# Performance work log

Measured on AMD Instinct MI355X. Metric: run time of the kernel, lower is better.

Reference implementation:

```python
import jax, jax.numpy as jnp
import numpy as np

D_MODEL = 96
EXPAND = 2.0
D_INNER = int(EXPAND * D_MODEL)  # 192
D_STATE = 1
DT_RANK = 6  # ceil(96/16)
K = 4
B, H, W = 4, 128, 128
L = H * W


def setup_inputs() -> dict:
    key = jax.random.key(0)
    ks = jax.random.split(key, 12)
    x = jax.random.normal(ks[0], (B, D_MODEL, H, W), dtype=jnp.float32)
    # 4 per-direction scan permutations of L and their inverses
    scan_ids = jnp.stack([jax.random.permutation(jax.random.fold_in(ks[1], k), L) for k in range(K)]).astype(jnp.int32)
    inverse_ids = jnp.argsort(scan_ids, axis=1).astype(jnp.int32)
    in_proj_w = jax.random.normal(ks[2], (D_INNER, D_MODEL), dtype=jnp.float32) * (1.0 / np.sqrt(D_MODEL))
    conv_w = jax.random.normal(ks[3], (D_INNER, 1, 3, 3), dtype=jnp.float32) * (1.0 / 3.0)
    conv_b = jax.random.normal(ks[4], (D_INNER,), dtype=jnp.float32) * 0.02
    x_proj_weight = jax.random.normal(ks[5], (K, DT_RANK + 2 * D_STATE, D_INNER), dtype=jnp.float32) * (1.0 / np.sqrt(D_INNER))
    dt_projs_weight = 0.1 * jax.random.uniform(ks[6], (K, D_INNER, DT_RANK), dtype=jnp.float32)
    dt_projs_bias = 0.1 * jax.random.uniform(ks[7], (K, D_INNER), dtype=jnp.float32)
    A_logs = jnp.zeros((K * D_INNER, D_STATE), dtype=jnp.float32)
    Ds = jnp.ones((K * D_INNER,), dtype=jnp.float32)
    out_proj_w = jax.random.normal(ks[8], (D_MODEL, D_INNER), dtype=jnp.float32) * (1.0 / np.sqrt(D_INNER))
    return {"x": x, "scan_ids": scan_ids, "inverse_ids": inverse_ids,
            "in_proj_w": in_proj_w, "conv_w": conv_w, "conv_b": conv_b,
            "x_proj_weight": x_proj_weight, "dt_projs_weight": dt_projs_weight,
            "dt_projs_bias": dt_projs_bias, "A_logs": A_logs, "Ds": Ds,
            "out_proj_w": out_proj_w}


def _selective_scan(u, delta, A, Bs, Cs, Ds, delta_bias):
    # u, delta: (B,K,D,L); A: (K,D,N); Bs, Cs: (B,K,N,L); Ds: (K,D); delta_bias: (K,D)
    delta = jax.nn.softplus(delta + delta_bias[None, :, :, None])  # (B,K,D,L)
    a = jnp.exp(delta[:, :, :, None, :] * A[None, :, :, :, None])  # (B,K,D,N,L)
    bu = delta[:, :, :, None, :] * Bs[:, :, None, :, :] * u[:, :, :, None, :]  # (B,K,D,N,L)

    def combine(lhs, rhs):
        aL, bL = lhs
        aR, bR = rhs
        return aR * aL, aR * bL + bR

    _, h = jax.lax.associative_scan(combine, (a, bu), axis=-1)  # h: (B,K,D,N,L)
    y = jnp.einsum('bknl,bkdnl->bkdl', Cs, h) + Ds[None, :, :, None] * u
    return y


def reference(x, scan_ids, inverse_ids, in_proj_w, conv_w, conv_b, x_proj_weight,
              dt_projs_weight, dt_projs_bias, A_logs, Ds, out_proj_w):
    Bsz, _, Hh, Ww = x.shape
    Ll = Hh * Ww
    # in_proj (1x1 conv == linear over channels)
    x = jnp.einsum('oc,bchw->bohw', in_proj_w, x)
    # depthwise 3x3 conv, padding SAME
    x = jax.lax.conv_general_dilated(x, conv_w, (1, 1), 'SAME',
                                     dimension_numbers=('NCHW', 'OIHW', 'NCHW'),
                                     feature_group_count=D_INNER)
    x = x + conv_b[None, :, None, None]
    x = jax.nn.silu(x)
    # 4-direction gather: (B,D,L) -> (B,K,D,L)
    xf = x.reshape(Bsz, D_INNER, Ll)
    xs = jnp.transpose(xf[:, :, scan_ids], (0, 2, 1, 3))  # (B,K,D,L)
    # input-dependent projections
    x_dbl = jnp.einsum('bkdl,kcd->bkcl', xs, x_proj_weight)
    dts, Bm, Cm = jnp.split(x_dbl, [DT_RANK, DT_RANK + D_STATE], axis=2)
    dts = jnp.einsum('bkrl,kdr->bkdl', dts, dt_projs_weight)
    A = -jnp.exp(A_logs.astype(jnp.float32)).reshape(K, D_INNER, D_STATE)
    ys = _selective_scan(xs.astype(jnp.float32), dts.astype(jnp.float32), A,
                         Bm.astype(jnp.float32), Cm.astype(jnp.float32),
                         Ds.astype(jnp.float32).reshape(K, D_INNER),
                         dt_projs_bias.astype(jnp.float32))  # (B,K,D,L)
    # inverse scatter per direction (gather with inverse permutation), then sum
    yinv = jnp.take_along_axis(ys, inverse_ids[None, :, None, :].astype(jnp.int32), axis=-1)
    y = jnp.sum(yinv, axis=1).reshape(Bsz, D_INNER, Hh, Ww)
    y = jax.nn.gelu(y)
    out = jnp.einsum('oc,bchw->bohw', out_proj_w, y)
    return out
```

## Files before the change

kernel.cpp:

```cpp
#include <hip/hip_runtime.h>
#include <math.h>

#define BATCH 4
#define HH 128
#define WWW 128
#define LLEN (HH*WWW)
#define CIN 96
#define DI 192
#define KDIR 4
#define NCH 512
#define PCH 32

__global__ __launch_bounds__(256) void k_inproj(const float* __restrict__ x,
                                                const float* __restrict__ w,
                                                float* __restrict__ t0) {
    __shared__ float xin[CIN * 64];
    __shared__ float wt[CIN * 65];
    int bid = blockIdx.x;
    int b = bid >> 8;
    int l0 = (bid & 255) << 6;
    int t = threadIdx.x;
    for (int i = 0; i < 24; ++i) {
        int idx = t + i * 256;
        int c = idx >> 6, l = idx & 63;
        xin[c * 64 + l] = x[((size_t)(b * CIN + c)) * LLEN + l0 + l];
    }
    int o_lane = t & 63;
    int lgrp = t >> 6;
    for (int ot = 0; ot < 3; ++ot) {
        __syncthreads();
        for (int i = 0; i < 24; ++i) {
            int idx = t + i * 256;
            int o = idx / 96, c = idx - o * 96;
            wt[c * 65 + o] = w[(ot * 64 + o) * 96 + c];
        }
        __syncthreads();
        float4 acc4[4];
        #pragma unroll
        for (int i = 0; i < 4; ++i) acc4[i] = make_float4(0.f, 0.f, 0.f, 0.f);
        int lb = lgrp * 16;
        for (int c = 0; c < CIN; ++c) {
            float wv = wt[c * 65 + o_lane];
            const float4* xv = reinterpret_cast<const float4*>(&xin[c * 64 + lb]);
            #pragma unroll
            for (int i = 0; i < 4; ++i) {
                float4 xx = xv[i];
                acc4[i].x += wv * xx.x; acc4[i].y += wv * xx.y;
                acc4[i].z += wv * xx.z; acc4[i].w += wv * xx.w;
            }
        }
        int o = ot * 64 + o_lane;
        #pragma unroll
        for (int i = 0; i < 4; ++i) {
            t0[((size_t)(b * LLEN) + l0 + lb + i * 4 + 0) * DI + o] = acc4[i].x;
            t0[((size_t)(b * LLEN) + l0 + lb + i * 4 + 1) * DI + o] = acc4[i].y;
            t0[((size_t)(b * LLEN) + l0 + lb + i * 4 + 2) * DI + o] = acc4[i].z;
            t0[((size_t)(b * LLEN) + l0 + lb + i * 4 + 3) * DI + o] = acc4[i].w;
        }
    }
}

__global__ __launch_bounds__(192) void k_dwconv(const float* __restrict__ t0,
                                                const float* __restrict__ cw,
                                                const float* __restrict__ cb,
                                                float* __restrict__ xf) {
    int bid = blockIdx.x;
    int wt = (bid & 15) << 3;
    int h  = (bid >> 4) & (HH - 1);
    int b  = bid >> 11;
    int d  = threadIdx.x;
    float acc[8];
    float bias = cb[d];
    #pragma unroll
    for (int j = 0; j < 8; ++j) acc[j] = bias;
    #pragma unroll
    for (int kh = 0; kh < 3; ++kh) {
        int hh = h + kh - 1;
        if (hh < 0 || hh >= HH) continue;
        float w0v = cw[d * 9 + kh * 3 + 0];
        float w1v = cw[d * 9 + kh * 3 + 1];
        float w2v = cw[d * 9 + kh * 3 + 2];
        const float* rowp = t0 + ((size_t)(b * LLEN) + hh * WWW) * DI + d;
        float v[10];
        #pragma unroll
        for (int j = 0; j < 10; ++j) {
            int ww = wt + j - 1;
            v[j] = (ww < 0 || ww >= WWW) ? 0.f : rowp[(size_t)ww * DI];
        }
        #pragma unroll
        for (int j = 0; j < 8; ++j)
            acc[j] += w0v * v[j] + w1v * v[j + 1] + w2v * v[j + 2];
    }
    size_t outbase = ((size_t)(b * LLEN) + h * WWW + wt) * DI + d;
    #pragma unroll
    for (int j = 0; j < 8; ++j) {
        float aa = acc[j];
        float s = aa * __builtin_amdgcn_rcpf(1.f + __expf(-aa));
        xf[outbase + (size_t)j * DI] = s;
    }
}

__global__ __launch_bounds__(256) void k_proj(const float* __restrict__ xf,
                                              const float* __restrict__ xpw,
                                              float* __restrict__ xdblp) {
    __shared__ float wl[32 * DI];
    __shared__ float part[4 * 32 * 33];
    int bid = blockIdx.x;
    int t = threadIdx.x;
    {
        const float4* wsrc = reinterpret_cast<const float4*>(xpw);
        float4* wdst = reinterpret_cast<float4*>(wl);
        #pragma unroll
        for (int i = 0; i < 6; ++i) wdst[t + i * 256] = wsrc[t + i * 256];
    }
    int p = t & 31, s = t >> 5;
    const float4* row = reinterpret_cast<const float4*>(
        xf + ((size_t)bid * 32 + p) * DI + s * 24);
    float4 v[6];
    #pragma unroll
    for (int j = 0; j < 6; ++j) v[j] = row[j];
    __syncthreads();
    float pd[32];
    #pragma unroll
    for (int ch = 0; ch < 32; ++ch) {
        const float4* w4 = reinterpret_cast<const float4*>(wl + ch * DI + s * 24);
        float a0 = 0.f;
        #pragma unroll
        for (int j = 0; j < 6; ++j) {
            float4 wv = w4[j];
            a0 += wv.x * v[j].x + wv.y * v[j].y + wv.z * v[j].z + wv.w * v[j].w;
        }
        pd[ch] = a0;
    }
    #pragma unroll
    for (int ch = 0; ch < 32; ++ch) pd[ch] += __shfl_xor(pd[ch], 32);
    if ((s & 1) == 0) {
        int wq = s >> 1;
        #pragma unroll
        for (int ch = 0; ch < 32; ++ch) part[(wq * 32 + p) * 33 + ch] = pd[ch];
    }
    __syncthreads();
    int pos = t >> 3, c4 = t & 7;
    float r[4];
    #pragma unroll
    for (int i = 0; i < 4; ++i) {
        int ch = c4 * 4 + i;
        r[i] = part[pos * 33 + ch] + part[(32 + pos) * 33 + ch] +
               part[(64 + pos) * 33 + ch] + part[(96 + pos) * 33 + ch];
    }
    reinterpret_cast<float4*>(xdblp + (size_t)bid * 1024)[t] =
        make_float4(r[0], r[1], r[2], r[3]);
}

__global__ __launch_bounds__(192) void k_scan1(const float* __restrict__ xf,
                                               const int* __restrict__ sids,
                                               const float* __restrict__ xdblp,
                                               const float* __restrict__ dtw,
                                               const float* __restrict__ dtb,
                                               const float* __restrict__ alog,
                                               float* __restrict__ cA,
                                               float* __restrict__ cB) {
    __shared__ float xdbl[PCH * 8];
    __shared__ int sid[PCH];
    int bid = blockIdx.x;
    int c = bid & (NCH - 1);
    int k = (bid >> 9) & 3;
    int b = bid >> 11;
    int t = threadIdx.x;
    if (t < PCH) sid[t] = sids[k * LLEN + c * PCH + t];
    __syncthreads();
    if (t < 64) {
        int p = t >> 1, half = t & 1;
        reinterpret_cast<float4*>(xdbl)[t] = *reinterpret_cast<const float4*>(
            xdblp + ((size_t)(b * LLEN) + sid[p]) * 32 + k * 8 + half * 4);
    }
    __syncthreads();
    int d = t;
    const float* ubase = xf + (size_t)(b * LLEN) * DI + d;
    float uv[PCH];
    #pragma unroll
    for (int p = 0; p < PCH; ++p) uv[p] = ubase[(size_t)sid[p] * DI];
    float wr[6];
    #pragma unroll
    for (int r = 0; r < 6; ++r) wr[r] = dtw[(k * DI + d) * 6 + r];
    float bias = dtb[k * DI + d];
    float A = -__expf(alog[k * DI + d]);
    float Ar = 1.f, Br = 0.f;
    const float4* xd4 = reinterpret_cast<const float4*>(xdbl);
    #pragma unroll
    for (int p = 0; p < PCH; ++p) {
        float4 x0 = xd4[p * 2], x1 = xd4[p * 2 + 1];
        float s = bias + wr[0] * x0.x + wr[1] * x0.y + wr[2] * x0.z +
                  wr[3] * x0.w + wr[4] * x1.x + wr[5] * x1.y;
        float delta = (s > 20.f) ? s : __logf(1.f + __expf(s));
        float a = __expf(delta * A);
        float bu = delta * x1.z * uv[p];
        Br = a * Br + bu;
        Ar *= a;
    }
    cA[(size_t)bid * DI + d] = Ar;
    cB[(size_t)bid * DI + d] = Br;
}

__global__ __launch_bounds__(192) void k_cs1(const float* __restrict__ cA,
                                             const float* __restrict__ cB,
                                             float* __restrict__ segA,
                                             float* __restrict__ segB) {
    int g = blockIdx.x;
    int d = threadIdx.x;
    size_t base = (size_t)g * 32 * DI + d;
    float A = 1.f, Bv = 0.f;
    for (int cc = 0; cc < 32; ++cc) {
        float a = cA[base + (size_t)cc * DI];
        float bb = cB[base + (size_t)cc * DI];
        Bv = a * Bv + bb;
        A *= a;
    }
    segA[(size_t)g * DI + d] = A;
    segB[(size_t)g * DI + d] = Bv;
}
__global__ __launch_bounds__(192) void k_cs2(const float* __restrict__ segA,
                                             const float* __restrict__ segB,
                                             float* __restrict__ hseg) {
    int bk = blockIdx.x;
    int d = threadIdx.x;
    float h = 0.f;
    for (int seg = 0; seg < 16; ++seg) {
        size_t idx = (size_t)(bk * 16 + seg) * DI + d;
        hseg[idx] = h;
        h = segA[idx] * h + segB[idx];
    }
}
__global__ __launch_bounds__(192) void k_cs3(const float* __restrict__ cA,
                                             float* __restrict__ cB,
                                             const float* __restrict__ hseg) {
    int g = blockIdx.x;
    int d = threadIdx.x;
    float h = hseg[(size_t)g * DI + d];
    size_t base = (size_t)g * 32 * DI + d;
    for (int cc = 0; cc < 32; ++cc) {
        size_t ix = base + (size_t)cc * DI;
        float a = cA[ix];
        float bb = cB[ix];
        cB[ix] = h;
        h = a * h + bb;
    }
}

template <bool ACCUM>
__global__ __launch_bounds__(192) void k_scan3(const float* __restrict__ xf,
                                               const int* __restrict__ sids,
                                               const float* __restrict__ dtw,
                                               const float* __restrict__ dtb,
                                               const float* __restrict__ alog,
                                               const float* __restrict__ dsv,
                                               const float* __restrict__ hin,
                                               const float* __restrict__ xdblp,
                                               float* __restrict__ y,
                                               int k) {
    __shared__ float xdbl[PCH * 8];
    __shared__ int sid[PCH];
    int bid = blockIdx.x;
    int c = bid & (NCH - 1);
    int b = bid >> 9;
    int t = threadIdx.x;
    size_t gidx = (size_t)((b * KDIR + k) * NCH + c);
    if (t < PCH) sid[t] = sids[k * LLEN + c * PCH + t];
    __syncthreads();
    if (t < 64) {
        int p = t >> 1, half = t & 1;
        reinterpret_cast<float4*>(xdbl)[t] = *reinterpret_cast<const float4*>(
            xdblp + ((size_t)(b * LLEN) + sid[p]) * 32 + k * 8 + half * 4);
    }
    __syncthreads();
    int d = t;
    const float* ubase = xf + (size_t)(b * LLEN) * DI + d;
    float* ybase = y + (size_t)(b * LLEN) * DI + d;
    float uv[PCH];
    #pragma unroll
    for (int p = 0; p < PCH; ++p) uv[p] = ubase[(size_t)sid[p] * DI];
    float yv[PCH];
    if (ACCUM) {
        #pragma unroll
        for (int p = 0; p < PCH; ++p) yv[p] = ybase[(size_t)sid[p] * DI];
    }
    float wr[6];
    #pragma unroll
    for (int r = 0; r < 6; ++r) wr[r] = dtw[(k * DI + d) * 6 + r];
    float bias = dtb[k * DI + d];
    float A = -__expf(alog[k * DI + d]);
    float Dv = dsv[k * DI + d];
    float h = hin[gidx * DI + d];
    const float4* xd4 = reinterpret_cast<const float4*>(xdbl);
    #pragma unroll
    for (int p = 0; p < PCH; ++p) {
        float4 x0 = xd4[p * 2], x1 = xd4[p * 2 + 1];
        float s = bias + wr[0] * x0.x + wr[1] * x0.y + wr[2] * x0.z +
                  wr[3] * x0.w + wr[4] * x1.x + wr[5] * x1.y;
        float delta = (s > 20.f) ? s : __logf(1.f + __expf(s));
        float a = __expf(delta * A);
        float bu = delta * x1.z * uv[p];
        h = a * h + bu;
        float ys = x1.w * h + Dv * uv[p];
        if (ACCUM) ys += yv[p];
        ybase[(size_t)sid[p] * DI] = ys;
    }
}

__global__ __launch_bounds__(256) void k_out(const float* __restrict__ y,
                                             const float* __restrict__ wo,
                                             float* __restrict__ out) {
    __shared__ float gy[DI * 65];
    int bid = blockIdx.x;
    int b = bid >> 8;
    int l0 = (bid & 255) << 6;
    int t = threadIdx.x;
    for (int i = 0; i < 48; ++i) {
        int idx = t + i * 256;
        int l = idx / DI;
        int cc = idx - l * DI;
        float v = y[((size_t)(b * LLEN) + l0 + l) * DI + cc];
        float z = 0.7978845608028654f * (v + 0.044715f * v * v * v);
        float e = __expf(2.f * z);
        float th = 1.f - 2.f * __builtin_amdgcn_rcpf(e + 1.f);
        gy[cc * 65 + l] = 0.5f * v * (1.f + th);
    }
    __syncthreads();
    int lq = t & 15, oh = t >> 4;
    float acc[6][4];
    #pragma unroll
    for (int i = 0; i < 6; ++i)
        #pragma unroll
        for (int e = 0; e < 4; ++e) acc[i][e] = 0.f;
    for (int cc = 0; cc < DI; cc += 4) {
        float4 wv[6];
        #pragma unroll
        for (int i = 0; i < 6; ++i)
            wv[i] = *reinterpret_cast<const float4*>(&wo[(oh * 6 + i) * DI + cc]);
        float g[4][4];
        #pragma unroll
        for (int el = 0; el < 4; ++el) {
            g[el][0] = gy[(cc + 0) * 65 + lq * 4 + el];
            g[el][1] = gy[(cc + 1) * 65 + lq * 4 + el];
            g[el][2] = gy[(cc + 2) * 65 + lq * 4 + el];
            g[el][3] = gy[(cc + 3) * 65 + lq * 4 + el];
        }
        #pragma unroll
        for (int i = 0; i < 6; ++i)
            #pragma unroll
            for (int el = 0; el < 4; ++el)
                acc[i][el] += wv[i].x * g[el][0] + wv[i].y * g[el][1] +
                              wv[i].z * g[el][2] + wv[i].w * g[el][3];
    }
    #pragma unroll
    for (int i = 0; i < 6; ++i) {
        int o = oh * 6 + i;
        float4 st = make_float4(acc[i][0], acc[i][1], acc[i][2], acc[i][3]);
        *reinterpret_cast<float4*>(&out[((size_t)(b * CIN) + o) * LLEN + l0 + lq * 4]) = st;
    }
}

extern "C" void kernel_launch(void* const* d_in, const int* in_sizes, int n_in,
                              void* d_out, int out_size, void* d_ws, size_t ws_size,
                              hipStream_t stream) {
    const float* x        = (const float*)d_in[0];
    const int*   scan_ids = (const int*)d_in[1];
    const float* in_proj_w = (const float*)d_in[3];
    const float* conv_w    = (const float*)d_in[4];
    const float* conv_b    = (const float*)d_in[5];
    const float* xpw       = (const float*)d_in[6];
    const float* dtw       = (const float*)d_in[7];
    const float* dtb       = (const float*)d_in[8];
    const float* alog      = (const float*)d_in[9];
    const float* dsv       = (const float*)d_in[10];
    const float* wo        = (const float*)d_in[11];
    float* out = (float*)d_out;

    float* ws = (float*)d_ws;
    const size_t NBL  = (size_t)BATCH * LLEN * DI;
    const size_t NCK  = (size_t)BATCH * KDIR * NCH * DI;
    const size_t NXD  = (size_t)BATCH * LLEN * 32;
    const size_t NSG  = (size_t)BATCH * KDIR * 16 * DI;
    float* t0    = ws;
    float* xf    = t0 + NBL;
    float* xdblp = xf + NBL;
    float* cA    = xdblp + NXD;
    float* cB    = cA + NCK;
    float* segA  = cB + NCK;
    float* segB  = segA + NSG;
    float* hseg  = segB + NSG;
    float* y     = t0;

    k_inproj<<<BATCH * 256, 256, 0, stream>>>(x, in_proj_w, t0);
    k_dwconv<<<BATCH * HH * 16, 192, 0, stream>>>(t0, conv_w, conv_b, xf);
    k_proj<<<(BATCH * LLEN) / 32, 256, 0, stream>>>(xf, xpw, xdblp);
    k_scan1<<<BATCH * KDIR * NCH, 192, 0, stream>>>(xf, scan_ids, xdblp, dtw, dtb,
                                                    alog, cA, cB);
    k_cs1<<<BATCH * KDIR * 16, 192, 0, stream>>>(cA, cB, segA, segB);
    k_cs2<<<BATCH * KDIR, 192, 0, stream>>>(segA, segB, hseg);
    k_cs3<<<BATCH * KDIR * 16, 192, 0, stream>>>(cA, cB, hseg);
    k_scan3<false><<<BATCH * NCH, 192, 0, stream>>>(xf, scan_ids, dtw, dtb,
                                                    alog, dsv, cB, xdblp, y, 0);
    for (int k = 1; k < KDIR; ++k)
        k_scan3<true><<<BATCH * NCH, 192, 0, stream>>>(xf, scan_ids, dtw, dtb,
                                                       alog, dsv, cB, xdblp, y, k);
    k_out<<<BATCH * 256, 256, 0, stream>>>(y, wo, out);
}
```

Before: 433.1 us.

## Compute input projection with bf16 MFMA after converting inputs and weights

The fp32 shared-memory FMA GEMM for the input projection is replaced with bf16 MFMA 16x16x32 instructions. Two new kernels first cast the weights and the activations to bf16, transposing x into a (B,L,C) row-major layout. The cast buffers reuse scratch regions (cA, segA) that later stages overwrite. In exchange, input-projection precision drops to bf16, and two extra launches plus an extra pass over x are added.

```diff
diff --git a/kernel.cpp b/kernel.cpp
--- a/kernel.cpp
+++ b/kernel.cpp
@@ -11,52 +11,67 @@
 #define NCH 512
 #define PCH 32
 
-__global__ __launch_bounds__(256) void k_inproj(const float* __restrict__ x,
-                                                const float* __restrict__ w,
+typedef __attribute__((ext_vector_type(8))) short bf16x8;
+typedef __attribute__((ext_vector_type(4))) float floatx4;
+
+__device__ inline unsigned pack_bf16(float a, float b) {
+    unsigned ua = __float_as_uint(a); ua = (ua + 0x7fffu + ((ua >> 16) & 1u)) >> 16;
+    unsigned ub = __float_as_uint(b); ub = (ub + 0x7fffu + ((ub >> 16) & 1u)) >> 16;
+    return ua | (ub << 16);
+}
+
+__global__ __launch_bounds__(256) void k_cvtw(const float* __restrict__ w,
+                                              unsigned* __restrict__ wb) {
+    int i = blockIdx.x * 256 + threadIdx.x;
+    float2 v = reinterpret_cast<const float2*>(w)[i];
+    wb[i] = pack_bf16(v.x, v.y);
+}
+
+__global__ __launch_bounds__(256) void k_cvt(const float* __restrict__ x,
+                                             unsigned short* __restrict__ xb) {
+    int g = blockIdx.x * 256 + threadIdx.x;
+    int b = g >> 14, l = g & (LLEN - 1);
+    const float* xp = x + (size_t)b * CIN * LLEN + l;
+    uint4* dst = reinterpret_cast<uint4*>(xb + (size_t)g * CIN);
+    #pragma unroll
+    for (int c0 = 0; c0 < CIN; c0 += 8) {
+        float v[8];
+        #pragma unroll
+        for (int j = 0; j < 8; ++j) v[j] = xp[(size_t)(c0 + j) * LLEN];
+        uint4 o;
+        o.x = pack_bf16(v[0], v[1]); o.y = pack_bf16(v[2], v[3]);
+        o.z = pack_bf16(v[4], v[5]); o.w = pack_bf16(v[6], v[7]);
+        dst[c0 >> 3] = o;
+    }
+}
+
+__global__ __launch_bounds__(256) void k_inproj(const unsigned short* __restrict__ xb,
+                                                const unsigned short* __restrict__ wb,
                                                 float* __restrict__ t0) {
-    __shared__ float xin[CIN * 64];
-    __shared__ float wt[CIN * 65];
-    int bid = blockIdx.x;
+    int bid = blockIdx.x;
+    int t = threadIdx.x;
+    int wv = t >> 6, lane = t & 63;
     int b = bid >> 8;
-    int l0 = (bid & 255) << 6;
-    int t = threadIdx.x;
-    for (int i = 0; i < 24; ++i) {
-        int idx = t + i * 256;
-        int c = idx >> 6, l = idx & 63;
-        xin[c * 64 + l] = x[((size_t)(b * CIN + c)) * LLEN + l0 + l];
-    }
-    int o_lane = t & 63;
-    int lgrp = t >> 6;
-    for (int ot = 0; ot < 3; ++ot) {
-        __syncthreads();
-        for (int i = 0; i < 24; ++i) {
-            int idx = t + i * 256;
-            int o = idx / 96, c = idx - o * 96;
-            wt[c * 65 + o] = w[(ot * 64 + o) * 96 + c];
-        }
-        __syncthreads();
-        float4 acc4[4];
-        #pragma unroll
-        for (int i = 0; i < 4; ++i) acc4[i] = make_float4(0.f, 0.f, 0.f, 0.f);
-        int lb = lgrp * 16;
-        for (int c = 0; c < CIN; ++c) {
-            float wv = wt[c * 65 + o_lane];
-            const float4* xv = reinterpret_cast<const float4*>(&xin[c * 64 + lb]);
-            #pragma unroll
-            for (int i = 0; i < 4; ++i) {
-                float4 xx = xv[i];
-                acc4[i].x += wv * xx.x; acc4[i].y += wv * xx.y;
-                acc4[i].z += wv * xx.z; acc4[i].w += wv * xx.w;
-            }
-        }
-        int o = ot * 64 + o_lane;
-        #pragma unroll
-        for (int i = 0; i < 4; ++i) {
-            t0[((size_t)(b * LLEN) + l0 + lb + i * 4 + 0) * DI + o] = acc4[i].x;
-            t0[((size_t)(b * LLEN) + l0 + lb + i * 4 + 1) * DI + o] = acc4[i].y;
-            t0[((size_t)(b * LLEN) + l0 + lb + i * 4 + 2) * DI + o] = acc4[i].z;
-            t0[((size_t)(b * LLEN) + l0 + lb + i * 4 + 3) * DI + o] = acc4[i].w;
-        }
+    int l0 = (bid & 255) * 64 + wv * 16;
+    int m = lane & 15, kg = lane >> 4;
+    const unsigned short* xrow = xb + ((size_t)(b * LLEN) + l0 + m) * CIN + kg * 8;
+    bf16x8 a0 = *reinterpret_cast<const bf16x8*>(xrow);
+    bf16x8 a1 = *reinterpret_cast<const bf16x8*>(xrow + 32);
+    bf16x8 a2 = *reinterpret_cast<const bf16x8*>(xrow + 64);
+    float* obase = t0 + ((size_t)(b * LLEN) + l0 + kg * 4) * DI + m;
+    #pragma unroll
+    for (int ot = 0; ot < 12; ++ot) {
+        const unsigned short* wrow = wb + (size_t)(ot * 16 + m) * CIN + kg * 8;
+        bf16x8 b0 = *reinterpret_cast<const bf16x8*>(wrow);
+        bf16x8 b1 = *reinterpret_cast<const bf16x8*>(wrow + 32);
+        bf16x8 b2 = *reinterpret_cast<const bf16x8*>(wrow + 64);
+        floatx4 acc = {0.f, 0.f, 0.f, 0.f};
+        acc = __builtin_amdgcn_mfma_f32_16x16x32_bf16(a0, b0, acc, 0, 0, 0);
+        acc = __builtin_amdgcn_mfma_f32_16x16x32_bf16(a1, b1, acc, 0, 0, 0);
+        acc = __builtin_amdgcn_mfma_f32_16x16x32_bf16(a2, b2, acc, 0, 0, 0);
+        #pragma unroll
+        for (int r = 0; r < 4; ++r)
+            obase[(size_t)r * DI + ot * 16] = acc[r];
     }
 }
 
@@ -390,8 +405,12 @@
     float* segB  = segA + NSG;
     float* hseg  = segB + NSG;
     float* y     = t0;
-
-    k_inproj<<<BATCH * 256, 256, 0, stream>>>(x, in_proj_w, t0);
+    unsigned short* Xb = reinterpret_cast<unsigned short*>(cA);
+    unsigned*       Wb = reinterpret_cast<unsigned*>(segA);
+
+    k_cvtw<<<36, 256, 0, stream>>>(in_proj_w, Wb);
+    k_cvt<<<256, 256, 0, stream>>>(x, Xb);
+    k_inproj<<<BATCH * 256, 256, 0, stream>>>(Xb, (const unsigned short*)Wb, t0);
     k_dwconv<<<BATCH * HH * 16, 192, 0, stream>>>(t0, conv_w, conv_b, xf);
     k_proj<<<(BATCH * LLEN) / 32, 256, 0, stream>>>(xf, xpw, xdblp);
     k_scan1<<<BATCH * KDIR * NCH, 192, 0, stream>>>(xf, scan_ids, xdblp, dtw, dtb,
```

After: 384.3 us. -11.3%, faster.
